# Kernel optimization log

Hardware: AMD Instinct MI355X
Metric: run time of the kernel (lower is better)

## Reference

```python
import jax, jax.numpy as jnp
import numpy as np

N = 16384
D_IN = 128
D_OUT = 128


def setup_inputs() -> dict:
    key = jax.random.key(0)
    k_adj, k_feat, k_neigh, k_w = jax.random.split(key, 4)
    adj = jax.random.uniform(k_adj, (N, N), dtype=jnp.float32)
    features = jax.random.normal(k_feat, (N, D_IN), dtype=jnp.float32)
    neigh_feats = jax.random.normal(k_neigh, (N, D_IN), dtype=jnp.float32)
    # xavier-uniform-ish init for Linear(2*D_IN -> D_OUT), weight stored [out, in] like torch
    limit = np.sqrt(2.0) * np.sqrt(6.0 / (2 * D_IN + D_OUT))
    W = jax.random.uniform(k_w, (D_OUT, 2 * D_IN), dtype=jnp.float32,
                           minval=-limit, maxval=limit)
    return {"adj": adj, "features": features, "neigh_feats": neigh_feats, "W": W}


def reference(adj, features, neigh_feats, W):
    # len(neigh_feats) == len(features) -> no fill_diagonal_ in the original.
    # neighbor aggregation with degree normalization (degree + 1)
    deg = jnp.sum(adj, axis=1, keepdims=True) + 1.0           # [N, 1]
    neigh_feature = (adj @ neigh_feats) / deg                  # [N, D_IN]
    data = jnp.concatenate([features, neigh_feature], axis=-1)  # [N, 2*D_IN]
    combined = data @ W.T                                      # [N, D_OUT]
    return combined
```

## Files before the change

### kernel.cpp

```cpp
#include <hip/hip_runtime.h>
#include <hip/hip_bf16.h>
#include <stdint.h>

#define NN 16384
#define BM 64
#define KHALF 8192
#define BKA 128
#define BKB 64
#define NG1 (KHALF / BKA)
#define NKT1 (KHALF / BKB)

typedef __attribute__((ext_vector_type(8))) short bf16x8;
typedef __attribute__((ext_vector_type(4))) float f32x4;
typedef __attribute__((ext_vector_type(4))) unsigned short u16x4;
typedef __attribute__((ext_vector_type(8))) unsigned short u16x8;
typedef __attribute__((ext_vector_type(4))) unsigned int u32x4;

__device__ __forceinline__ unsigned short f2bf(float f) {
    uint32_t u = __builtin_bit_cast(uint32_t, f);
    u += 0x7fffu + ((u >> 16) & 1u);
    return (unsigned short)(u >> 16);
}

__global__ __launch_bounds__(256) void prep_transpose(const float* __restrict__ src,
                                                      unsigned short* __restrict__ dstT) {
    __shared__ unsigned short tl[128][66];
    const int t = threadIdx.x;
    const int r0 = blockIdx.x * 64;
#pragma unroll
    for (int i = 0; i < 8; ++i) {
        int idx = i * 256 + t;
        int r = idx >> 5;
        int s = idx & 31;
        f32x4 v = *(const f32x4*)(src + (size_t)(r0 + r) * 128 + s * 4);
#pragma unroll
        for (int j = 0; j < 4; ++j) tl[s * 4 + j][r] = f2bf(v[j]);
    }
    __syncthreads();
    const int c = t >> 1;
    const int half = t & 1;
#pragma unroll
    for (int j = 0; j < 4; ++j) {
        u16x8 p;
#pragma unroll
        for (int e = 0; e < 8; ++e) p[e] = tl[c][half * 32 + j * 8 + e];
        *(u16x8*)(dstT + (size_t)c * NN + r0 + half * 32 + j * 8) = p;
    }
}

#define MFMA16(a, b, c) __builtin_amdgcn_mfma_f32_16x16x32_bf16(a, b, c, 0, 0, 0)

#define BARRIER() do {                                          \
    asm volatile("s_waitcnt lgkmcnt(0)" ::: "memory");          \
    __builtin_amdgcn_s_barrier();                               \
    __builtin_amdgcn_sched_barrier(0);                          \
} while (0)

__global__ __launch_bounds__(256, 2) void sage_partial(
    const float* __restrict__ adj,
    const unsigned short* __restrict__ neighT,
    float* __restrict__ S01,
    float* __restrict__ deg01)
{
    __shared__ __align__(16) char smem[65536];
    char* aL = smem;
    char* bL = smem + 32768;

    const int t = threadIdx.x;
    const int lane = t & 63;
    const int wv = t >> 6;
    const int mt = wv >> 1;
    const int nt = wv & 1;
    const size_t row0 = (size_t)(blockIdx.x >> 1) * BM;
    const int half = blockIdx.x & 1;
    const size_t koff = (size_t)half * KHALF;

    const int ra0 = t >> 3;
    const int asl = t & 7;
    const float* aG0 = adj + (row0 + ra0) * (size_t)NN + koff + asl * 4;
    const float* aG1 = aG0 + (size_t)32 * NN;

    int awz[8];
#pragma unroll
    for (int i = 0; i < 8; ++i) {
        int row = (i < 4) ? ra0 : (ra0 + 32);
        int j = i & 3;
        awz[i] = row * 256 + ((j * 64 + asl * 8) ^ ((row & 7) << 4));
    }

    const int br0 = t >> 3;
    const int bcs = (t & 7) * 8;
    const unsigned short* bG = neighT + (size_t)br0 * NN + koff + bcs;
    int bwb[4];
#pragma unroll
    for (int i = 0; i < 4; ++i) {
        int br = br0 + 32 * i;
        bwb[i] = (br * 128 + bcs * 2) ^ ((br & 7) << 4);
    }

    f32x4 acc[2][4];
#pragma unroll
    for (int i = 0; i < 2; ++i)
#pragma unroll
        for (int j = 0; j < 4; ++j) acc[i][j] = (f32x4){0.f, 0.f, 0.f, 0.f};

    float dsum[2] = {0.f, 0.f};

    f32x4 arA[8];
    u32x4 br_[4];

#define ISSUE_A(G) do {                                                       \
    _Pragma("unroll")                                                         \
    for (int i = 0; i < 8; ++i) {                                             \
        const float* p = (i < 4 ? aG0 : aG1) + (size_t)(G) * BKA + (i & 3) * 32; \
        arA[i] = __builtin_nontemporal_load((const f32x4*)p);                 \
    }                                                                         \
} while (0)

#define ISSUE_B(KT) do {                                                      \
    _Pragma("unroll")                                                         \
    for (int i = 0; i < 4; ++i)                                               \
        br_[i] = *(const u32x4*)(bG + (size_t)(32 * i) * NN +                 \
                                 (size_t)(KT) * BKB);                         \
} while (0)

#define STAGE_A(DST) do {                                                     \
    _Pragma("unroll")                                                         \
    for (int i = 0; i < 8; ++i) {                                             \
        f32x4 v = arA[i];                                                     \
        dsum[i >> 2] += (v[0] + v[1]) + (v[2] + v[3]);                        \
        u16x4 p; p.x = f2bf(v[0]); p.y = f2bf(v[1]);                          \
        p.z = f2bf(v[2]); p.w = f2bf(v[3]);                                   \
        *(u16x4*)((DST) + awz[i]) = p;                                        \
    }                                                                         \
} while (0)

#define STAGE_B(BUF) do {                                                     \
    char* bW = bL + (BUF) * 16384;                                            \
    _Pragma("unroll")                                                         \
    for (int i = 0; i < 4; ++i)                                               \
        *(u32x4*)(bW + bwb[i]) = br_[i];                                      \
} while (0)

#define COMPUTE(ABASE, SUB, BBUF) do {                                        \
    const char* aB = (ABASE);                                                 \
    const char* bB = bL + (BBUF) * 16384;                                     \
    _Pragma("unroll")                                                         \
    for (int ks = 0; ks < 2; ++ks) {                                          \
        bf16x8 af[2], bfr[4];                                                 \
        _Pragma("unroll")                                                     \
        for (int ms = 0; ms < 2; ++ms) {                                      \
            int r = mt * 32 + ms * 16 + (lane & 15);                          \
            int off = r * 256 + (((SUB) * 128 + ks * 64 + (lane >> 4) * 16)   \
                      ^ ((r & 7) << 4));                                      \
            af[ms] = *(const bf16x8*)(aB + off);                              \
        }                                                                     \
        _Pragma("unroll")                                                     \
        for (int ns = 0; ns < 4; ++ns) {                                      \
            int c = nt * 64 + ns * 16 + (lane & 15);                          \
            int off = c * 128 + ((ks * 64 + (lane >> 4) * 16)                 \
                      ^ ((c & 7) << 4));                                      \
            bfr[ns] = *(const bf16x8*)(bB + off);                             \
        }                                                                     \
        _Pragma("unroll")                                                     \
        for (int ms = 0; ms < 2; ++ms)                                        \
            _Pragma("unroll")                                                 \
            for (int ns = 0; ns < 4; ++ns)                                    \
                acc[ms][ns] = MFMA16(af[ms], bfr[ns], acc[ms][ns]);           \
    }                                                                         \
} while (0)

    ISSUE_B(0);
    ISSUE_A(0);
    STAGE_B(0);
    STAGE_A(aL);
    BARRIER();

    for (int g = 0; g < NG1; ++g) {
        char* aCur = aL + (g & 1) * 16384;
        char* aNxt = aL + ((g & 1) ^ 1) * 16384;
#pragma unroll
        for (int s = 0; s < 2; ++s) {
            const int kt = g * 2 + s;
            if (kt + 1 < NKT1) ISSUE_B(kt + 1);
            if (s == 0 && g + 1 < NG1) ISSUE_A(g + 1);
            COMPUTE(aCur, s, kt & 1);
            if (kt + 1 < NKT1) STAGE_B((kt + 1) & 1);
            if (s == 1 && g + 1 < NG1) STAGE_A(aNxt);
            BARRIER();
        }
    }

    dsum[0] += __shfl_xor(dsum[0], 1, 64);
    dsum[0] += __shfl_xor(dsum[0], 2, 64);
    dsum[0] += __shfl_xor(dsum[0], 4, 64);
    dsum[1] += __shfl_xor(dsum[1], 1, 64);
    dsum[1] += __shfl_xor(dsum[1], 2, 64);
    dsum[1] += __shfl_xor(dsum[1], 4, 64);
    float* degp = deg01 + (size_t)half * NN;
    if (asl == 0) {
        degp[row0 + ra0] = dsum[0];
        degp[row0 + ra0 + 32] = dsum[1];
    }

    float* Sp = S01 + (size_t)half * NN * 128;
#pragma unroll
    for (int ms = 0; ms < 2; ++ms)
#pragma unroll
        for (int ns = 0; ns < 4; ++ns)
#pragma unroll
            for (int j = 0; j < 4; ++j) {
                int r = mt * 32 + ms * 16 + (lane >> 4) * 4 + j;
                int c = nt * 64 + ns * 16 + (lane & 15);
                Sp[(row0 + r) * 128 + c] = acc[ms][ns][j];
            }
}

__global__ __launch_bounds__(256) void sage_epilogue(
    const float* __restrict__ feat,
    const float* __restrict__ W,
    const float* __restrict__ S01,
    const float* __restrict__ deg01,
    float* __restrict__ out)
{
    __shared__ __align__(16) char smem[33024];
    char* dL = smem;
    float* degp = (float*)(smem + 32768);

    const int t = threadIdx.x;
    const int lane = t & 63;
    const int wv = t >> 6;
    const int mt = wv >> 1;
    const int nt = wv & 1;
    const size_t row0 = (size_t)blockIdx.x * BM;

    if (t < 64) degp[t] = deg01[row0 + t] + deg01[NN + row0 + t];

#pragma unroll
    for (int i = 0; i < 8; ++i) {
        int idx = i * 256 + t;
        int r = idx >> 5;
        int s = idx & 31;
        f32x4 v = *(const f32x4*)(feat + (row0 + r) * 128 + s * 4);
        u16x4 p; p.x = f2bf(v[0]); p.y = f2bf(v[1]); p.z = f2bf(v[2]); p.w = f2bf(v[3]);
        int off = (r * 512 + s * 8) ^ ((r & 7) << 4);
        *(u16x4*)(dL + off) = p;
    }
    __syncthreads();

#pragma unroll
    for (int i = 0; i < 8; ++i) {
        int idx = i * 256 + t;
        int r = idx >> 5;
        int s = idx & 31;
        size_t o = (row0 + r) * 128 + s * 4;
        f32x4 v0 = *(const f32x4*)(S01 + o);
        f32x4 v1 = *(const f32x4*)(S01 + (size_t)NN * 128 + o);
        float inv = 1.0f / (degp[r] + 1.0f);
        u16x4 p;
        p.x = f2bf((v0[0] + v1[0]) * inv); p.y = f2bf((v0[1] + v1[1]) * inv);
        p.z = f2bf((v0[2] + v1[2]) * inv); p.w = f2bf((v0[3] + v1[3]) * inv);
        int off = (r * 512 + 256 + s * 8) ^ ((r & 7) << 4);
        *(u16x4*)(dL + off) = p;
    }
    __syncthreads();

    f32x4 acc2[2][4];
#pragma unroll
    for (int i = 0; i < 2; ++i)
#pragma unroll
        for (int j = 0; j < 4; ++j) acc2[i][j] = (f32x4){0.f, 0.f, 0.f, 0.f};

#pragma unroll
    for (int ks = 0; ks < 8; ++ks) {
        bf16x8 af[2], bfr[4];
#pragma unroll
        for (int ms = 0; ms < 2; ++ms) {
            int r = mt * 32 + ms * 16 + (lane & 15);
            int off = r * 512 + ((ks * 64 + (lane >> 4) * 16) ^ ((r & 7) << 4));
            af[ms] = *(const bf16x8*)(dL + off);
        }
#pragma unroll
        for (int ns = 0; ns < 4; ++ns) {
            int c = nt * 64 + ns * 16 + (lane & 15);
            int k0 = ks * 32 + (lane >> 4) * 8;
            f32x4 w0 = *(const f32x4*)(W + (size_t)c * 256 + k0);
            f32x4 w1 = *(const f32x4*)(W + (size_t)c * 256 + k0 + 4);
            u16x8 p;
            p[0] = f2bf(w0[0]); p[1] = f2bf(w0[1]); p[2] = f2bf(w0[2]); p[3] = f2bf(w0[3]);
            p[4] = f2bf(w1[0]); p[5] = f2bf(w1[1]); p[6] = f2bf(w1[2]); p[7] = f2bf(w1[3]);
            bfr[ns] = __builtin_bit_cast(bf16x8, p);
        }
#pragma unroll
        for (int ms = 0; ms < 2; ++ms)
#pragma unroll
            for (int ns = 0; ns < 4; ++ns)
                acc2[ms][ns] = MFMA16(af[ms], bfr[ns], acc2[ms][ns]);
    }

#pragma unroll
    for (int ms = 0; ms < 2; ++ms)
#pragma unroll
        for (int ns = 0; ns < 4; ++ns)
#pragma unroll
            for (int j = 0; j < 4; ++j) {
                int r = mt * 32 + ms * 16 + (lane >> 4) * 4 + j;
                int c = nt * 64 + ns * 16 + (lane & 15);
                out[(row0 + r) * 128 + c] = acc2[ms][ns][j];
            }
}

extern "C" void kernel_launch(void* const* d_in, const int* in_sizes, int n_in,
                              void* d_out, int out_size, void* d_ws, size_t ws_size,
                              hipStream_t stream) {
    const float* adj = (const float*)d_in[0];
    const float* feat = (const float*)d_in[1];
    const float* neigh = (const float*)d_in[2];
    const float* W = (const float*)d_in[3];
    float* out = (float*)d_out;

    unsigned short* neighT = (unsigned short*)d_ws;
    float* deg01 = (float*)((char*)d_ws + (size_t)4 * 1024 * 1024);
    float* S01 = (float*)((char*)d_ws + (size_t)8 * 1024 * 1024);

    prep_transpose<<<NN / 64, 256, 0, stream>>>(neigh, neighT);
    sage_partial<<<(NN / BM) * 2, 256, 0, stream>>>(adj, neighT, S01, deg01);
    sage_epilogue<<<NN / BM, 256, 0, stream>>>(feat, W, S01, deg01, out);
}
```

Before: 224.9 us.

## Load neighbor tiles directly into LDS via global_load_lds DMA

Replaces the register-staged load of the bf16 neighbor-feature B tiles with global_load_lds, which writes global data straight into shared memory. The XOR swizzle moves to the source address, and the main loop is unrolled by hand with explicit vmcnt waits and barriers. The goal is to free VGPRs and drop the LDS store instructions for B. In exchange, synchronisation is stricter: the vmcnt(0) waits at the end of each group may serialize the A and B loads more than before.

```diff
diff --git a/kernel.cpp b/kernel.cpp
--- a/kernel.cpp
+++ b/kernel.cpp
@@ -16,6 +16,9 @@
 typedef __attribute__((ext_vector_type(8))) unsigned short u16x8;
 typedef __attribute__((ext_vector_type(4))) unsigned int u32x4;
 
+typedef __attribute__((address_space(1))) const unsigned int gu32;
+typedef __attribute__((address_space(3))) unsigned int lu32;
+
 __device__ __forceinline__ unsigned short f2bf(float f) {
     uint32_t u = __builtin_bit_cast(uint32_t, f);
     u += 0x7fffu + ((u >> 16) & 1u);
@@ -49,12 +52,6 @@
 }
 
 #define MFMA16(a, b, c) __builtin_amdgcn_mfma_f32_16x16x32_bf16(a, b, c, 0, 0, 0)
-
-#define BARRIER() do {                                          \
-    asm volatile("s_waitcnt lgkmcnt(0)" ::: "memory");          \
-    __builtin_amdgcn_s_barrier();                               \
-    __builtin_amdgcn_sched_barrier(0);                          \
-} while (0)
 
 __global__ __launch_bounds__(256, 2) void sage_partial(
     const float* __restrict__ adj,
@@ -88,15 +85,9 @@
         awz[i] = row * 256 + ((j * 64 + asl * 8) ^ ((row & 7) << 4));
     }
 
-    const int br0 = t >> 3;
-    const int bcs = (t & 7) * 8;
-    const unsigned short* bG = neighT + (size_t)br0 * NN + koff + bcs;
-    int bwb[4];
-#pragma unroll
-    for (int i = 0; i < 4; ++i) {
-        int br = br0 + 32 * i;
-        bwb[i] = (br * 128 + bcs * 2) ^ ((br & 7) << 4);
-    }
+    const int bc = t >> 3;
+    const int bslot = (t & 7) ^ (bc & 7);
+    const unsigned short* bG2 = neighT + (size_t)bc * NN + koff + bslot * 8;
 
     f32x4 acc[2][4];
 #pragma unroll
@@ -107,7 +98,6 @@
     float dsum[2] = {0.f, 0.f};
 
     f32x4 arA[8];
-    u32x4 br_[4];
 
 #define ISSUE_A(G) do {                                                       \
     _Pragma("unroll")                                                         \
@@ -117,11 +107,15 @@
     }                                                                         \
 } while (0)
 
-#define ISSUE_B(KT) do {                                                      \
+#define ISSUE_B_DMA(KT, BUF) do {                                             \
+    char* bW = bL + (BUF) * 16384;                                            \
     _Pragma("unroll")                                                         \
-    for (int i = 0; i < 4; ++i)                                               \
-        br_[i] = *(const u32x4*)(bG + (size_t)(32 * i) * NN +                 \
-                                 (size_t)(KT) * BKB);                         \
+    for (int i = 0; i < 4; ++i) {                                             \
+        const unsigned short* gp = bG2 + (size_t)(i * 32) * NN +              \
+                                   (size_t)(KT) * BKB;                        \
+        void* lp = bW + i * 4096 + wv * 1024;                                 \
+        __builtin_amdgcn_global_load_lds((gu32*)gp, (lu32*)lp, 16, 0, 0);     \
+    }                                                                         \
 } while (0)
 
 #define STAGE_A(DST) do {                                                     \
@@ -133,13 +127,6 @@
         p.z = f2bf(v[2]); p.w = f2bf(v[3]);                                   \
         *(u16x4*)((DST) + awz[i]) = p;                                        \
     }                                                                         \
-} while (0)
-
-#define STAGE_B(BUF) do {                                                     \
-    char* bW = bL + (BUF) * 16384;                                            \
-    _Pragma("unroll")                                                         \
-    for (int i = 0; i < 4; ++i)                                               \
-        *(u32x4*)(bW + bwb[i]) = br_[i];                                      \
 } while (0)
 
 #define COMPUTE(ABASE, SUB, BBUF) do {                                        \
@@ -170,25 +157,36 @@
     }                                                                         \
 } while (0)
 
-    ISSUE_B(0);
+    ISSUE_B_DMA(0, 0);
+    __builtin_amdgcn_sched_barrier(0);
     ISSUE_A(0);
-    STAGE_B(0);
     STAGE_A(aL);
-    BARRIER();
+    asm volatile("s_waitcnt vmcnt(0) lgkmcnt(0)" ::: "memory");
+    __builtin_amdgcn_s_barrier();
+    __builtin_amdgcn_sched_barrier(0);
 
     for (int g = 0; g < NG1; ++g) {
         char* aCur = aL + (g & 1) * 16384;
         char* aNxt = aL + ((g & 1) ^ 1) * 16384;
-#pragma unroll
-        for (int s = 0; s < 2; ++s) {
-            const int kt = g * 2 + s;
-            if (kt + 1 < NKT1) ISSUE_B(kt + 1);
-            if (s == 0 && g + 1 < NG1) ISSUE_A(g + 1);
-            COMPUTE(aCur, s, kt & 1);
-            if (kt + 1 < NKT1) STAGE_B((kt + 1) & 1);
-            if (s == 1 && g + 1 < NG1) STAGE_A(aNxt);
-            BARRIER();
-        }
+        const bool more = (g + 1 < NG1);
+        const int kt = 2 * g;
+
+        ISSUE_B_DMA(kt + 1, (kt + 1) & 1);
+        __builtin_amdgcn_sched_barrier(0);
+        if (more) ISSUE_A(g + 1);
+        COMPUTE(aCur, 0, kt & 1);
+        if (more) asm volatile("s_waitcnt vmcnt(8)" ::: "memory");
+        else      asm volatile("s_waitcnt vmcnt(0)" ::: "memory");
+        __builtin_amdgcn_s_barrier();
+        __builtin_amdgcn_sched_barrier(0);
+
+        if (more) ISSUE_B_DMA(kt + 2, (kt + 2) & 1);
+        __builtin_amdgcn_sched_barrier(0);
+        COMPUTE(aCur, 1, (kt + 1) & 1);
+        if (more) STAGE_A(aNxt);
+        asm volatile("s_waitcnt vmcnt(0) lgkmcnt(0)" ::: "memory");
+        __builtin_amdgcn_s_barrier();
+        __builtin_amdgcn_sched_barrier(0);
     }
 
     dsum[0] += __shfl_xor(dsum[0], 1, 64);
```

Measured after the change: 195.5 us. 1.15x faster.
